# Performance work log

Measured on AMD Instinct MI355X. Metric: run time of the kernel, lower is better.

Reference implementation:

```python
import jax, jax.numpy as jnp
import numpy as np

N = 100000   # nodes
E = 3200000  # edges (avg degree 32)
WIDTH = 32
DEPTH = 4


def setup_inputs() -> dict:
    key = jax.random.key(0)
    ks = jax.random.split(key, 12)
    def lin(k, fan_in, fan_out):
        s = 1.0 / np.sqrt(fan_in)
        kw, kb = jax.random.split(k)
        W = jax.random.uniform(kw, (fan_in, fan_out), jnp.float32, -s, s)
        b = jax.random.uniform(kb, (fan_out,), jnp.float32, -s, s)
        return W, b
    x = jax.random.normal(ks[0], (N, 3), jnp.float32)
    edge_index = jax.random.randint(ks[1], (2, E), 0, N, jnp.int64)
    fc1_w, fc1_b = lin(ks[2], 3, WIDTH)
    w1, b1 = lin(ks[3], WIDTH, 2 * WIDTH)
    w2, b2 = lin(ks[4], 2 * WIDTH, 2 * WIDTH)
    w3, b3 = lin(ks[5], 2 * WIDTH, WIDTH)
    fc2_w, fc2_b = lin(ks[6], WIDTH, 1)
    return {"x": x, "edge_index": edge_index,
            "fc1_w": fc1_w, "fc1_b": fc1_b,
            "w1": w1, "b1": b1, "w2": w2, "b2": b2, "w3": w3, "b3": b3,
            "fc2_w": fc2_w, "fc2_b": fc2_b}


def reference(x, edge_index, fc1_w, fc1_b, w1, b1, w2, b2, w3, b3, fc2_w, fc2_b):
    # GCNConv semantics: add self-loops, symmetric degree normalization,
    # linear transform then normalized scatter-add aggregation.
    loops = jnp.arange(N, dtype=edge_index.dtype)
    src = jnp.concatenate([edge_index[0], loops])  # [E+N]
    dst = jnp.concatenate([edge_index[1], loops])  # [E+N]
    deg = jax.ops.segment_sum(jnp.ones_like(dst, dtype=x.dtype), dst, num_segments=N)
    dinv = jnp.where(deg > 0, jax.lax.rsqrt(deg), 0.0)
    norm = (dinv[src] * dinv[dst])[:, None]  # [E+N, 1]

    def gcn(h, W, b):
        m = (h @ W)[src] * norm                      # gather + scale
        return jax.ops.segment_sum(m, dst, num_segments=N) + b  # scatter-add

    h = x @ fc1_w + fc1_b
    for _ in range(DEPTH):
        h = jax.nn.relu(gcn(h, w1, b1))
        h = jax.nn.relu(gcn(h, w2, b2))
        h = jax.nn.relu(gcn(h, w3, b3))
    return h @ fc2_w + fc2_b
```

## Files before the change

kernel.cpp:

```cpp
#include <hip/hip_runtime.h>
#include <hip/hip_fp16.h>

constexpr int NN = 100000;
constexpr int EE = 3200000;
constexpr int BLOCK = 256;
constexpr int NBINS = 782;
constexpr int BINCAP = 5120;
constexpr int CHUNK = 4096;
constexpr int NCHB = (EE + CHUNK - 1) / CHUNK;
constexpr int NCLS = 512;

typedef _Float16 h2v __attribute__((ext_vector_type(2)));

__device__ __forceinline__ unsigned int pack2(float x, float y) {
  return __builtin_bit_cast(unsigned int, __floats2half2_rn(x, y));
}

__device__ __forceinline__ float dot2acc(float acc, unsigned int a, unsigned int b) {
#if __has_builtin(__builtin_amdgcn_fdot2)
  return __builtin_amdgcn_fdot2(__builtin_bit_cast(h2v, a),
                                __builtin_bit_cast(h2v, b), acc, false);
#else
  float2 fa = __half22float2(__builtin_bit_cast(__half2, a));
  float2 fb = __half22float2(__builtin_bit_cast(__half2, b));
  return fmaf(fa.x, fb.x, fmaf(fa.y, fb.y, acc));
#endif
}

__device__ __forceinline__ float addLo(float acc, unsigned int bits) {
#if __has_builtin(__builtin_amdgcn_fdot2)
  h2v h = __builtin_bit_cast(h2v, bits);
  const h2v eLo = {(_Float16)1.0f, (_Float16)0.0f};
  return __builtin_amdgcn_fdot2(h, eLo, acc, false);
#else
  __half2 hh = __builtin_bit_cast(__half2, bits);
  return acc + __half2float(hh.x);
#endif
}

__device__ __forceinline__ float addHi(float acc, unsigned int bits) {
#if __has_builtin(__builtin_amdgcn_fdot2)
  h2v h = __builtin_bit_cast(h2v, bits);
  const h2v eHi = {(_Float16)0.0f, (_Float16)1.0f};
  return __builtin_amdgcn_fdot2(h, eHi, acc, false);
#else
  __half2 hh = __builtin_bit_cast(__half2, bits);
  return acc + __half2float(hh.y);
#endif
}

__global__ __launch_bounds__(256) void k_binA(const int* __restrict__ src,
                                              const int* __restrict__ dst,
                                              int* __restrict__ cursor,
                                              unsigned int* __restrict__ binarr) {
  __shared__ int cnt[1024];
  __shared__ int off[1024];
  __shared__ int gbase[NBINS];
  __shared__ int ssc[256];
  __shared__ unsigned int stag[CHUNK];
  int tid = threadIdx.x;
  int base = blockIdx.x * CHUNK;
  for (int i = tid; i < 1024; i += 256) cnt[i] = 0;
  __syncthreads();
  for (int i = tid; i < CHUNK; i += 256) {
    int e = base + i;
    if (e < EE) atomicAdd(&cnt[dst[e] >> 7], 1);
  }
  __syncthreads();
  int t4 = tid * 4;
  int s0 = cnt[t4], s1 = cnt[t4 + 1], s2 = cnt[t4 + 2], s3 = cnt[t4 + 3];
  int tsum = s0 + s1 + s2 + s3;
  ssc[tid] = tsum;
  __syncthreads();
  for (int o = 1; o < 256; o <<= 1) {
    int x = (tid >= o) ? ssc[tid - o] : 0;
    __syncthreads();
    ssc[tid] += x;
    __syncthreads();
  }
  int ex = ssc[tid] - tsum;
  off[t4] = ex;
  off[t4 + 1] = ex + s0;
  off[t4 + 2] = ex + s0 + s1;
  off[t4 + 3] = ex + s0 + s1 + s2;
  __syncthreads();
  for (int b = tid; b < NBINS; b += 256) {
    int c = cnt[b];
    gbase[b] = c ? atomicAdd(&cursor[b], c) : 0;
    cnt[b] = off[b];
  }
  __syncthreads();
  for (int i = tid; i < CHUNK; i += 256) {
    int e = base + i;
    if (e < EE) {
      int d = dst[e];
      int b = d >> 7;
      int p = atomicAdd(&cnt[b], 1);
      stag[p] = ((unsigned int)src[e] << 7) | (unsigned int)(d & 127);
    }
  }
  __syncthreads();
  int total = (base + CHUNK <= EE) ? CHUNK : (EE - base);
  for (int i = tid; i < total; i += 256) {
    int lo = 0, hi = NBINS - 1;
    while (lo < hi) {
      int mid = (lo + hi + 1) >> 1;
      if (off[mid] <= i) lo = mid;
      else hi = mid - 1;
    }
    binarr[(size_t)lo * BINCAP + gbase[lo] + (i - off[lo])] = stag[i];
  }
}

__global__ __launch_bounds__(256) void k_degcnt(const unsigned int* __restrict__ binarr,
                                                const int* __restrict__ cursor,
                                                int* __restrict__ deg,
                                                int* __restrict__ bh) {
  __shared__ int cnt[128];
  __shared__ int lh[NCLS];
  int b = blockIdx.x, tid = threadIdx.x;
  if (tid < 128) cnt[tid] = 0;
  for (int i = tid; i < NCLS; i += 256) lh[i] = 0;
  __syncthreads();
  int n = cursor[b];
  const unsigned int* p = binarr + (size_t)b * BINCAP;
  for (int i = tid; i < n; i += 256) atomicAdd(&cnt[p[i] & 127], 1);
  __syncthreads();
  int node = b * 128 + tid;
  if (tid < 128 && node < NN) {
    int d = cnt[tid] < NCLS ? cnt[tid] : NCLS - 1;
    deg[node] = d;
    atomicAdd(&lh[d], 1);
  }
  __syncthreads();
  for (int i = tid; i < NCLS; i += 256) bh[(size_t)i * NBINS + b] = lh[i];
}

__global__ __launch_bounds__(256) void k_rowscan(int* __restrict__ bh,
                                                 int* __restrict__ tot) {
  int wid = (blockIdx.x * 256 + threadIdx.x) >> 6;
  int lane = threadIdx.x & 63;
  if (wid >= NCLS) return;
  int* row = bh + (size_t)wid * NBINS;
  int run = 0;
  for (int base = 0; base < NBINS; base += 64) {
    int i = base + lane;
    int v = (i < NBINS) ? row[i] : 0;
    int s = v;
#pragma unroll
    for (int o = 1; o < 64; o <<= 1) {
      int x = __shfl_up(s, o);
      if (lane >= o) s += x;
    }
    if (i < NBINS) row[i] = run + s - v;
    run += __shfl(s, 63);
  }
  if (lane == 0) tot[wid] = run;
}

__global__ __launch_bounds__(NCLS) void k_clsscan(const int* __restrict__ tot,
                                                  int* __restrict__ nodestart,
                                                  int* __restrict__ edgebase) {
  __shared__ int sn[NCLS], se[NCLS];
  int t = threadIdx.x;
  int v = tot[t];
  int e0 = v * t;
  sn[t] = v;
  se[t] = e0;
  __syncthreads();
  for (int o = 1; o < NCLS; o <<= 1) {
    int a = 0, b = 0;
    if (t >= o) { a = sn[t - o]; b = se[t - o]; }
    __syncthreads();
    if (t >= o) { sn[t] += a; se[t] += b; }
    __syncthreads();
  }
  nodestart[t] = sn[t] - v;
  edgebase[t] = se[t] - e0;
}

__global__ __launch_bounds__(256) void k_place2(const int* __restrict__ deg,
                                                const int* __restrict__ bh,
                                                const int* __restrict__ nodestart,
                                                const int* __restrict__ edgebase,
                                                int* __restrict__ perm,
                                                int* __restrict__ invp,
                                                int* __restrict__ rowptr2,
                                                float* __restrict__ dinv2) {
  __shared__ int lcur[NCLS];
  int tid = threadIdx.x, b = blockIdx.x;
  for (int i = tid; i < NCLS; i += 256)
    lcur[i] = nodestart[i] + bh[(size_t)i * NBINS + b];
  __syncthreads();
  int n = b * 128 + tid;
  if (tid >= 128 || n >= NN) return;
  int d = deg[n];
  int nid = atomicAdd(&lcur[d], 1);
  perm[nid] = n;
  invp[n] = nid;
  int idx = nid - nodestart[d];
  rowptr2[nid] = edgebase[d] + idx * d;
  dinv2[nid] = rsqrtf((float)(d + 1));
  if (n == 0) rowptr2[NN] = EE;
}

__global__ __launch_bounds__(256) void k_binB2(const unsigned int* __restrict__ binarr,
                                               const int* __restrict__ cursor,
                                               const int* __restrict__ invp,
                                               const int* __restrict__ rowptr2,
                                               int* __restrict__ col2) {
  __shared__ unsigned int stag[BINCAP];
  __shared__ unsigned int stag2[BINCAP];
  __shared__ int cnt[1024];
  __shared__ unsigned short off16[1024];
  __shared__ int nbase[128];
  __shared__ int ssc[256];
  int b = blockIdx.x, tid = threadIdx.x;
  int n = cursor[b];
  const unsigned int* p = binarr + (size_t)b * BINCAP;
  for (int i = tid; i < 1024; i += 256) cnt[i] = 0;
  int node = b * 128 + tid;
  if (tid < 128) nbase[tid] = (node < NN) ? rowptr2[invp[node]] : 0;
  __syncthreads();
  for (int i = tid; i < n; i += 256) {
    unsigned int e = p[i];
    unsigned int s = (unsigned int)invp[e >> 7];
    stag[i] = (s << 7) | (e & 127u);
    atomicAdd(&cnt[((e & 127u) << 3) | (s >> 14)], 1);
  }
  __syncthreads();
  int t4 = tid * 4;
  int s0 = cnt[t4], s1 = cnt[t4 + 1], s2 = cnt[t4 + 2], s3 = cnt[t4 + 3];
  int tsum = s0 + s1 + s2 + s3;
  ssc[tid] = tsum;
  __syncthreads();
  for (int o = 1; o < 256; o <<= 1) {
    int x = (tid >= o) ? ssc[tid - o] : 0;
    __syncthreads();
    ssc[tid] += x;
    __syncthreads();
  }
  int ex = ssc[tid] - tsum;
  off16[t4] = (unsigned short)ex;
  off16[t4 + 1] = (unsigned short)(ex + s0);
  off16[t4 + 2] = (unsigned short)(ex + s0 + s1);
  off16[t4 + 3] = (unsigned short)(ex + s0 + s1 + s2);
  cnt[t4] = ex;
  cnt[t4 + 1] = ex + s0;
  cnt[t4 + 2] = ex + s0 + s1;
  cnt[t4 + 3] = ex + s0 + s1 + s2;
  __syncthreads();
  for (int i = tid; i < n; i += 256) {
    unsigned int en = stag[i];
    int key = (int)(((en & 127u) << 3) | ((en >> 7) >> 14));
    int pos = atomicAdd(&cnt[key], 1);
    stag2[pos] = en;
  }
  __syncthreads();
  for (int i = tid; i < n; i += 256) {
    unsigned int en = stag2[i];
    int dl = (int)(en & 127u);
    col2[nbase[dl] + (i - (int)off16[dl << 3])] = (int)(en >> 7);
  }
}

__global__ __launch_bounds__(BLOCK) void k_fc1(const float* __restrict__ x,
                                               __half* __restrict__ t0,
                                               const float* __restrict__ W,
                                               const float* __restrict__ b,
                                               const float* __restrict__ dinv,
                                               const int* __restrict__ perm) {
  __shared__ float Ws[3 * 32];
  __shared__ float bs[32];
  int tid = threadIdx.x;
  if (tid < 96) Ws[tid] = W[tid];
  if (tid < 32) bs[tid] = b[tid];
  __syncthreads();
  int node = blockIdx.x * 8 + (tid >> 5);
  int f = tid & 31;
  if (node >= NN) return;
  int on = perm[node];
  float x0 = x[on * 3], x1 = x[on * 3 + 1], x2 = x[on * 3 + 2];
  float v = fmaf(x0, Ws[f], fmaf(x1, Ws[32 + f], fmaf(x2, Ws[64 + f], bs[f])));
  t0[node * 32 + f] = __float2half(v * dinv[node]);
}

__global__ __launch_bounds__(BLOCK) void k_A(const uint2* __restrict__ t0,
                                             __half2* __restrict__ t1,
                                             const int* __restrict__ rowptr,
                                             const int* __restrict__ col,
                                             const float* __restrict__ dinv,
                                             const float* __restrict__ W1,
                                             const float* __restrict__ b1) {
  __shared__ unsigned int W1p[16 * 64];
  __shared__ float b1s[64];
  __shared__ unsigned int Hs2[32 * 17];
  int tid = threadIdx.x;
  for (int i = tid; i < 16 * 64; i += BLOCK) {
    int k2 = i >> 6, j = i & 63;
    W1p[i] = pack2(W1[(2 * k2) * 64 + j], W1[(2 * k2 + 1) * 64 + j]);
  }
  if (tid < 64) b1s[tid] = b1[tid];
  __syncthreads();

  int tile = (int)gridDim.x - 1 - (int)blockIdx.x;
  {
    int c = tid & 7, slot = tid >> 3;
    int node = tile * 32 + slot;
    uint2 raw = t0[(size_t)node * 8 + c];
    float a0 = 0.f, a1 = 0.f, a2 = 0.f, a3 = 0.f;
    a0 = addLo(a0, raw.x); a1 = addHi(a1, raw.x);
    a2 = addLo(a2, raw.y); a3 = addHi(a3, raw.y);
    int beg = rowptr[node], end = rowptr[node + 1];
#pragma unroll 8
    for (int e = beg; e < end; ++e) {
      uint2 r = t0[(size_t)col[e] * 8 + c];
      a0 = addLo(a0, r.x); a1 = addHi(a1, r.x);
      a2 = addLo(a2, r.y); a3 = addHi(a3, r.y);
    }
    float dv = dinv[node];
    Hs2[slot * 17 + 2 * c] = pack2(a0 * dv, a1 * dv);
    Hs2[slot * 17 + 2 * c + 1] = pack2(a2 * dv, a3 * dv);
  }
  __syncthreads();
  {
    int n = tid >> 3, c8 = tid & 7;
    int node = tile * 32 + n;
    float a[8];
#pragma unroll
    for (int j = 0; j < 8; ++j) a[j] = b1s[c8 * 8 + j];
#pragma unroll
    for (int k2 = 0; k2 < 16; ++k2) {
      unsigned int h = Hs2[n * 17 + k2];
#pragma unroll
      for (int jj = 0; jj < 8; ++jj)
        a[jj] = dot2acc(a[jj], h, W1p[k2 * 64 + c8 * 8 + jj]);
    }
    float dv = dinv[node];
    __half2* o = t1 + (size_t)node * 32 + c8 * 4;
#pragma unroll
    for (int jj = 0; jj < 4; ++jj)
      o[jj] = __float22half2_rn(make_float2(fmaxf(a[2 * jj], 0.f) * dv,
                                            fmaxf(a[2 * jj + 1], 0.f) * dv));
  }
}

__global__ __launch_bounds__(BLOCK) void k_C(const uint2* __restrict__ t1,
                                             __half2* __restrict__ t3,
                                             const int* __restrict__ rowptr,
                                             const int* __restrict__ col,
                                             const float* __restrict__ dinv,
                                             const float* __restrict__ W2,
                                             const float* __restrict__ b2,
                                             const float* __restrict__ W3) {
  __shared__ unsigned int W2p[32 * 64];
  __shared__ unsigned int W3p[32 * 32];
  __shared__ float b2s[64];
  __shared__ unsigned int H2p[16 * 33];
  __shared__ unsigned int G1p[16 * 33];
  int tid = threadIdx.x;
  for (int i = tid; i < 32 * 64; i += BLOCK) {
    int k2 = i >> 6, j = i & 63;
    W2p[i] = pack2(W2[(2 * k2) * 64 + j], W2[(2 * k2 + 1) * 64 + j]);
  }
  for (int i = tid; i < 32 * 32; i += BLOCK) {
    int k2 = i >> 5, j = i & 31;
    W3p[i] = pack2(W3[(2 * k2) * 32 + j], W3[(2 * k2 + 1) * 32 + j]);
  }
  if (tid < 64) b2s[tid] = b2[tid];
  __syncthreads();

  int tile = (int)gridDim.x - 1 - (int)blockIdx.x;
  {
    int c = tid & 15, slot = tid >> 4;
    int node = tile * 16 + slot;
    uint2 raw = t1[(size_t)node * 16 + c];
    float a0 = 0.f, a1 = 0.f, a2 = 0.f, a3 = 0.f;
    a0 = addLo(a0, raw.x); a1 = addHi(a1, raw.x);
    a2 = addLo(a2, raw.y); a3 = addHi(a3, raw.y);
    int beg = rowptr[node], end = rowptr[node + 1];
#pragma unroll 8
    for (int e = beg; e < end; ++e) {
      uint2 r = t1[(size_t)col[e] * 16 + c];
      a0 = addLo(a0, r.x); a1 = addHi(a1, r.x);
      a2 = addLo(a2, r.y); a3 = addHi(a3, r.y);
    }
    float dv = dinv[node];
    H2p[slot * 33 + 2 * c] = pack2(a0 * dv, a1 * dv);
    H2p[slot * 33 + 2 * c + 1] = pack2(a2 * dv, a3 * dv);
  }
  __syncthreads();
  {
    int n = tid >> 4, q = tid & 15;
    float a[4];
#pragma unroll
    for (int j = 0; j < 4; ++j) a[j] = b2s[q * 4 + j];
#pragma unroll
    for (int k2 = 0; k2 < 32; ++k2) {
      unsigned int h = H2p[n * 33 + k2];
#pragma unroll
      for (int jj = 0; jj < 4; ++jj)
        a[jj] = dot2acc(a[jj], h, W2p[k2 * 64 + q * 4 + jj]);
    }
    G1p[n * 33 + q * 2] = pack2(fmaxf(a[0], 0.f), fmaxf(a[1], 0.f));
    G1p[n * 33 + q * 2 + 1] = pack2(fmaxf(a[2], 0.f), fmaxf(a[3], 0.f));
  }
  __syncthreads();
  {
    int n = tid >> 4, c16 = tid & 15;
    int node = tile * 16 + n;
    float a0 = 0.f, a1 = 0.f;
#pragma unroll
    for (int k2 = 0; k2 < 32; ++k2) {
      unsigned int g = G1p[n * 33 + k2];
      a0 = dot2acc(a0, g, W3p[k2 * 32 + 2 * c16]);
      a1 = dot2acc(a1, g, W3p[k2 * 32 + 2 * c16 + 1]);
    }
    float dv = dinv[node];
    t3[(size_t)node * 16 + c16] = __float22half2_rn(make_float2(a0 * dv, a1 * dv));
  }
}

template <bool FINAL>
__global__ __launch_bounds__(BLOCK) void k_D(const uint2* __restrict__ t3,
                                             uint2* __restrict__ t0n,
                                             float* __restrict__ out,
                                             const int* __restrict__ rowptr,
                                             const int* __restrict__ col,
                                             const float* __restrict__ dinv,
                                             const float* __restrict__ b3,
                                             const float* __restrict__ fc2w,
                                             const float* __restrict__ fc2b,
                                             const int* __restrict__ perm) {
  int tid = threadIdx.x;
  int c = tid & 7, slot = tid >> 3;
  int tile = (int)gridDim.x - 1 - (int)blockIdx.x;
  int node = tile * 32 + slot;
  uint2 raw = t3[(size_t)node * 8 + c];
  float a0 = 0.f, a1 = 0.f, a2 = 0.f, a3 = 0.f;
  a0 = addLo(a0, raw.x); a1 = addHi(a1, raw.x);
  a2 = addLo(a2, raw.y); a3 = addHi(a3, raw.y);
  int beg = rowptr[node], end = rowptr[node + 1];
#pragma unroll 8
  for (int e = beg; e < end; ++e) {
    uint2 r = t3[(size_t)col[e] * 8 + c];
    a0 = addLo(a0, r.x); a1 = addHi(a1, r.x);
    a2 = addLo(a2, r.y); a3 = addHi(a3, r.y);
  }
  float dv = dinv[node];
  float h0 = fmaxf(fmaf(a0, dv, b3[4 * c]), 0.f);
  float h1 = fmaxf(fmaf(a1, dv, b3[4 * c + 1]), 0.f);
  float h2 = fmaxf(fmaf(a2, dv, b3[4 * c + 2]), 0.f);
  float h3 = fmaxf(fmaf(a3, dv, b3[4 * c + 3]), 0.f);
  if (!FINAL) {
    uint2 w;
    w.x = pack2(h0 * dv, h1 * dv);
    w.y = pack2(h2 * dv, h3 * dv);
    t0n[(size_t)node * 8 + c] = w;
  } else {
    float part = fmaf(h0, fc2w[4 * c],
                 fmaf(h1, fc2w[4 * c + 1],
                 fmaf(h2, fc2w[4 * c + 2], h3 * fc2w[4 * c + 3])));
#pragma unroll
    for (int off = 4; off > 0; off >>= 1) part += __shfl_down(part, off, 8);
    if (c == 0) out[perm[node]] = part + fc2b[0];
  }
}

extern "C" void kernel_launch(void* const* d_in, const int* in_sizes, int n_in,
                              void* d_out, int out_size, void* d_ws, size_t ws_size,
                              hipStream_t stream) {
  const float* x = (const float*)d_in[0];
  const int* ei = (const int*)d_in[1];
  const int* esrc = ei;
  const int* edst = ei + EE;
  const float* fc1_w = (const float*)d_in[2];
  const float* fc1_b = (const float*)d_in[3];
  const float* w1 = (const float*)d_in[4];
  const float* b1 = (const float*)d_in[5];
  const float* w2 = (const float*)d_in[6];
  const float* b2 = (const float*)d_in[7];
  const float* w3 = (const float*)d_in[8];
  const float* b3 = (const float*)d_in[9];
  const float* fc2_w = (const float*)d_in[10];
  const float* fc2_b = (const float*)d_in[11];

  char* p = (char*)d_ws;
  auto carve = [&](size_t bytes) {
    void* r = (void*)p;
    p += (bytes + 255) & ~(size_t)255;
    return r;
  };
  int* cursor = (int*)carve(NBINS * sizeof(int));
  int* nodestart = (int*)carve(NCLS * sizeof(int));
  int* edgebase = (int*)carve(NCLS * sizeof(int));
  int* tot = (int*)carve(NCLS * sizeof(int));
  int* deg = (int*)carve(NN * sizeof(int));
  int* bh = (int*)carve((size_t)NCLS * NBINS * sizeof(int));
  unsigned int* binarr = (unsigned int*)carve((size_t)NBINS * BINCAP * 4);
  int* rowptr2 = (int*)carve((NN + 1) * sizeof(int));
  int* col2 = (int*)carve(EE * sizeof(int));
  int* perm = (int*)carve(NN * sizeof(int));
  int* invp = (int*)carve(NN * sizeof(int));
  float* dinv2 = (float*)carve(NN * sizeof(float));
  __half* t32a = (__half*)carve((size_t)NN * 32 * sizeof(__half));
  __half* t64 = (__half*)carve((size_t)NN * 64 * sizeof(__half));
  __half* t32b = (__half*)carve((size_t)NN * 32 * sizeof(__half));

  hipMemsetAsync(cursor, 0, NBINS * sizeof(int), stream);

  k_binA<<<NCHB, 256, 0, stream>>>(esrc, edst, cursor, binarr);
  k_degcnt<<<NBINS, 256, 0, stream>>>(binarr, cursor, deg, bh);
  k_rowscan<<<(NCLS * 64 + 255) / 256, 256, 0, stream>>>(bh, tot);
  k_clsscan<<<1, NCLS, 0, stream>>>(tot, nodestart, edgebase);
  k_place2<<<NBINS, 256, 0, stream>>>(deg, bh, nodestart, edgebase, perm, invp,
                                      rowptr2, dinv2);
  k_binB2<<<NBINS, 256, 0, stream>>>(binarr, cursor, invp, rowptr2, col2);

  k_fc1<<<NN / 8, BLOCK, 0, stream>>>(x, t32a, fc1_w, fc1_b, dinv2, perm);

  for (int it = 0; it < 4; ++it) {
    k_A<<<NN / 32, BLOCK, 0, stream>>>((const uint2*)t32a, (__half2*)t64,
                                       rowptr2, col2, dinv2, w1, b1);
    k_C<<<NN / 16, BLOCK, 0, stream>>>((const uint2*)t64, (__half2*)t32b,
                                       rowptr2, col2, dinv2, w2, b2, w3);
    if (it < 3) {
      k_D<false><<<NN / 32, BLOCK, 0, stream>>>(
          (const uint2*)t32b, (uint2*)t32a, nullptr, rowptr2, col2, dinv2, b3,
          nullptr, nullptr, nullptr);
    } else {
      k_D<true><<<NN / 32, BLOCK, 0, stream>>>(
          (const uint2*)t32b, nullptr, (float*)d_out, rowptr2, col2, dinv2, b3,
          fc2_w, fc2_b, perm);
    }
  }
}
```

Before: 638.5 us.

## Use 16-byte gathers with split-edge halves in aggregation kernels and simplify binning

The three aggregation kernels now gather each neighbour row with uint4 (16-byte) loads instead of uint2. Each node's edge list is split across two thread groups that take alternating edges, and their partial sums are combined with a cross-lane shuffle. This is meant to cut the number of load instructions per edge and raise memory-level parallelism in the gather-bound loops. Separately, k_binA moves to 512 threads, records each staged edge's bin id in shared memory so the binary search can go away, and merges the cursor atomics into the scan step. The cost is more accumulator registers, extra shuffles, and possible imbalance between the two halves on odd-degree nodes.

```diff
diff --git a/kernel.cpp b/kernel.cpp
--- a/kernel.cpp
+++ b/kernel.cpp
@@ -49,66 +49,65 @@
 #endif
 }
 
-__global__ __launch_bounds__(256) void k_binA(const int* __restrict__ src,
+#define ACC8(r)                                                     \
+  a0 = addLo(a0, (r).x); a1 = addHi(a1, (r).x);                     \
+  a2 = addLo(a2, (r).y); a3 = addHi(a3, (r).y);                     \
+  a4 = addLo(a4, (r).z); a5 = addHi(a5, (r).z);                     \
+  a6 = addLo(a6, (r).w); a7 = addHi(a7, (r).w)
+
+__global__ __launch_bounds__(512) void k_binA(const int* __restrict__ src,
                                               const int* __restrict__ dst,
                                               int* __restrict__ cursor,
                                               unsigned int* __restrict__ binarr) {
   __shared__ int cnt[1024];
   __shared__ int off[1024];
   __shared__ int gbase[NBINS];
-  __shared__ int ssc[256];
+  __shared__ int ssc[512];
   __shared__ unsigned int stag[CHUNK];
+  __shared__ unsigned short binid[CHUNK];
   int tid = threadIdx.x;
   int base = blockIdx.x * CHUNK;
-  for (int i = tid; i < 1024; i += 256) cnt[i] = 0;
-  __syncthreads();
-  for (int i = tid; i < CHUNK; i += 256) {
+  for (int i = tid; i < 1024; i += 512) cnt[i] = 0;
+  __syncthreads();
+  for (int i = tid; i < CHUNK; i += 512) {
     int e = base + i;
     if (e < EE) atomicAdd(&cnt[dst[e] >> 7], 1);
   }
   __syncthreads();
-  int t4 = tid * 4;
-  int s0 = cnt[t4], s1 = cnt[t4 + 1], s2 = cnt[t4 + 2], s3 = cnt[t4 + 3];
-  int tsum = s0 + s1 + s2 + s3;
+  int t2 = tid * 2;
+  int s0 = cnt[t2], s1 = cnt[t2 + 1];
+  int tsum = s0 + s1;
   ssc[tid] = tsum;
   __syncthreads();
-  for (int o = 1; o < 256; o <<= 1) {
+  for (int o = 1; o < 512; o <<= 1) {
     int x = (tid >= o) ? ssc[tid - o] : 0;
     __syncthreads();
     ssc[tid] += x;
     __syncthreads();
   }
   int ex = ssc[tid] - tsum;
-  off[t4] = ex;
-  off[t4 + 1] = ex + s0;
-  off[t4 + 2] = ex + s0 + s1;
-  off[t4 + 3] = ex + s0 + s1 + s2;
-  __syncthreads();
-  for (int b = tid; b < NBINS; b += 256) {
-    int c = cnt[b];
-    gbase[b] = c ? atomicAdd(&cursor[b], c) : 0;
-    cnt[b] = off[b];
-  }
-  __syncthreads();
-  for (int i = tid; i < CHUNK; i += 256) {
+  off[t2] = ex;
+  off[t2 + 1] = ex + s0;
+  cnt[t2] = ex;
+  cnt[t2 + 1] = ex + s0;
+  if (t2 < NBINS) gbase[t2] = s0 ? atomicAdd(&cursor[t2], s0) : 0;
+  if (t2 + 1 < NBINS) gbase[t2 + 1] = s1 ? atomicAdd(&cursor[t2 + 1], s1) : 0;
+  __syncthreads();
+  for (int i = tid; i < CHUNK; i += 512) {
     int e = base + i;
     if (e < EE) {
       int d = dst[e];
       int b = d >> 7;
       int p = atomicAdd(&cnt[b], 1);
       stag[p] = ((unsigned int)src[e] << 7) | (unsigned int)(d & 127);
+      binid[p] = (unsigned short)b;
     }
   }
   __syncthreads();
   int total = (base + CHUNK <= EE) ? CHUNK : (EE - base);
-  for (int i = tid; i < total; i += 256) {
-    int lo = 0, hi = NBINS - 1;
-    while (lo < hi) {
-      int mid = (lo + hi + 1) >> 1;
-      if (off[mid] <= i) lo = mid;
-      else hi = mid - 1;
-    }
-    binarr[(size_t)lo * BINCAP + gbase[lo] + (i - off[lo])] = stag[i];
+  for (int i = tid; i < total; i += 512) {
+    int b = binid[i];
+    binarr[(size_t)b * BINCAP + gbase[b] + (i - off[b])] = stag[i];
   }
 }
 
@@ -285,7 +284,7 @@
   t0[node * 32 + f] = __float2half(v * dinv[node]);
 }
 
-__global__ __launch_bounds__(BLOCK) void k_A(const uint2* __restrict__ t0,
+__global__ __launch_bounds__(BLOCK) void k_A(const uint4* __restrict__ t0,
                                              __half2* __restrict__ t1,
                                              const int* __restrict__ rowptr,
                                              const int* __restrict__ col,
@@ -305,22 +304,33 @@
 
   int tile = (int)gridDim.x - 1 - (int)blockIdx.x;
   {
-    int c = tid & 7, slot = tid >> 3;
+    int c = tid & 3;
+    int half = (tid >> 2) & 1;
+    int slot = tid >> 3;
     int node = tile * 32 + slot;
-    uint2 raw = t0[(size_t)node * 8 + c];
     float a0 = 0.f, a1 = 0.f, a2 = 0.f, a3 = 0.f;
-    a0 = addLo(a0, raw.x); a1 = addHi(a1, raw.x);
-    a2 = addLo(a2, raw.y); a3 = addHi(a3, raw.y);
+    float a4 = 0.f, a5 = 0.f, a6 = 0.f, a7 = 0.f;
+    if (half == 0) {
+      uint4 raw = t0[(size_t)node * 4 + c];
+      ACC8(raw);
+    }
     int beg = rowptr[node], end = rowptr[node + 1];
-#pragma unroll 8
-    for (int e = beg; e < end; ++e) {
-      uint2 r = t0[(size_t)col[e] * 8 + c];
-      a0 = addLo(a0, r.x); a1 = addHi(a1, r.x);
-      a2 = addLo(a2, r.y); a3 = addHi(a3, r.y);
-    }
-    float dv = dinv[node];
-    Hs2[slot * 17 + 2 * c] = pack2(a0 * dv, a1 * dv);
-    Hs2[slot * 17 + 2 * c + 1] = pack2(a2 * dv, a3 * dv);
+#pragma unroll 4
+    for (int e = beg + half; e < end; e += 2) {
+      uint4 r = t0[(size_t)col[e] * 4 + c];
+      ACC8(r);
+    }
+    a0 += __shfl_xor(a0, 4); a1 += __shfl_xor(a1, 4);
+    a2 += __shfl_xor(a2, 4); a3 += __shfl_xor(a3, 4);
+    a4 += __shfl_xor(a4, 4); a5 += __shfl_xor(a5, 4);
+    a6 += __shfl_xor(a6, 4); a7 += __shfl_xor(a7, 4);
+    if (half == 0) {
+      float dv = dinv[node];
+      Hs2[slot * 17 + 4 * c] = pack2(a0 * dv, a1 * dv);
+      Hs2[slot * 17 + 4 * c + 1] = pack2(a2 * dv, a3 * dv);
+      Hs2[slot * 17 + 4 * c + 2] = pack2(a4 * dv, a5 * dv);
+      Hs2[slot * 17 + 4 * c + 3] = pack2(a6 * dv, a7 * dv);
+    }
   }
   __syncthreads();
   {
@@ -345,7 +355,7 @@
   }
 }
 
-__global__ __launch_bounds__(BLOCK) void k_C(const uint2* __restrict__ t1,
+__global__ __launch_bounds__(BLOCK) void k_C(const uint4* __restrict__ t1,
                                              __half2* __restrict__ t3,
                                              const int* __restrict__ rowptr,
                                              const int* __restrict__ col,
@@ -372,22 +382,33 @@
 
   int tile = (int)gridDim.x - 1 - (int)blockIdx.x;
   {
-    int c = tid & 15, slot = tid >> 4;
+    int c = tid & 7;
+    int half = (tid >> 3) & 1;
+    int slot = tid >> 4;
     int node = tile * 16 + slot;
-    uint2 raw = t1[(size_t)node * 16 + c];
     float a0 = 0.f, a1 = 0.f, a2 = 0.f, a3 = 0.f;
-    a0 = addLo(a0, raw.x); a1 = addHi(a1, raw.x);
-    a2 = addLo(a2, raw.y); a3 = addHi(a3, raw.y);
+    float a4 = 0.f, a5 = 0.f, a6 = 0.f, a7 = 0.f;
+    if (half == 0) {
+      uint4 raw = t1[(size_t)node * 8 + c];
+      ACC8(raw);
+    }
     int beg = rowptr[node], end = rowptr[node + 1];
-#pragma unroll 8
-    for (int e = beg; e < end; ++e) {
-      uint2 r = t1[(size_t)col[e] * 16 + c];
-      a0 = addLo(a0, r.x); a1 = addHi(a1, r.x);
-      a2 = addLo(a2, r.y); a3 = addHi(a3, r.y);
-    }
-    float dv = dinv[node];
-    H2p[slot * 33 + 2 * c] = pack2(a0 * dv, a1 * dv);
-    H2p[slot * 33 + 2 * c + 1] = pack2(a2 * dv, a3 * dv);
+#pragma unroll 4
+    for (int e = beg + half; e < end; e += 2) {
+      uint4 r = t1[(size_t)col[e] * 8 + c];
+      ACC8(r);
+    }
+    a0 += __shfl_xor(a0, 8); a1 += __shfl_xor(a1, 8);
+    a2 += __shfl_xor(a2, 8); a3 += __shfl_xor(a3, 8);
+    a4 += __shfl_xor(a4, 8); a5 += __shfl_xor(a5, 8);
+    a6 += __shfl_xor(a6, 8); a7 += __shfl_xor(a7, 8);
+    if (half == 0) {
+      float dv = dinv[node];
+      H2p[slot * 33 + 4 * c] = pack2(a0 * dv, a1 * dv);
+      H2p[slot * 33 + 4 * c + 1] = pack2(a2 * dv, a3 * dv);
+      H2p[slot * 33 + 4 * c + 2] = pack2(a4 * dv, a5 * dv);
+      H2p[slot * 33 + 4 * c + 3] = pack2(a6 * dv, a7 * dv);
+    }
   }
   __syncthreads();
   {
@@ -422,8 +443,8 @@
 }
 
 template <bool FINAL>
-__global__ __launch_bounds__(BLOCK) void k_D(const uint2* __restrict__ t3,
-                                             uint2* __restrict__ t0n,
+__global__ __launch_bounds__(BLOCK) void k_D(const uint4* __restrict__ t3,
+                                             uint4* __restrict__ t0n,
                                              float* __restrict__ out,
                                              const int* __restrict__ rowptr,
                                              const int* __restrict__ col,
@@ -433,37 +454,56 @@
                                              const float* __restrict__ fc2b,
                                              const int* __restrict__ perm) {
   int tid = threadIdx.x;
-  int c = tid & 7, slot = tid >> 3;
+  int c = tid & 3;
+  int half = (tid >> 2) & 1;
+  int slot = tid >> 3;
   int tile = (int)gridDim.x - 1 - (int)blockIdx.x;
   int node = tile * 32 + slot;
-  uint2 raw = t3[(size_t)node * 8 + c];
   float a0 = 0.f, a1 = 0.f, a2 = 0.f, a3 = 0.f;
-  a0 = addLo(a0, raw.x); a1 = addHi(a1, raw.x);
-  a2 = addLo(a2, raw.y); a3 = addHi(a3, raw.y);
+  float a4 = 0.f, a5 = 0.f, a6 = 0.f, a7 = 0.f;
+  if (half == 0) {
+    uint4 raw = t3[(size_t)node * 4 + c];
+    ACC8(raw);
+  }
   int beg = rowptr[node], end = rowptr[node + 1];
-#pragma unroll 8
-  for (int e = beg; e < end; ++e) {
-    uint2 r = t3[(size_t)col[e] * 8 + c];
-    a0 = addLo(a0, r.x); a1 = addHi(a1, r.x);
-    a2 = addLo(a2, r.y); a3 = addHi(a3, r.y);
-  }
+#pragma unroll 4
+  for (int e = beg + half; e < end; e += 2) {
+    uint4 r = t3[(size_t)col[e] * 4 + c];
+    ACC8(r);
+  }
+  a0 += __shfl_xor(a0, 4); a1 += __shfl_xor(a1, 4);
+  a2 += __shfl_xor(a2, 4); a3 += __shfl_xor(a3, 4);
+  a4 += __shfl_xor(a4, 4); a5 += __shfl_xor(a5, 4);
+  a6 += __shfl_xor(a6, 4); a7 += __shfl_xor(a7, 4);
   float dv = dinv[node];
-  float h0 = fmaxf(fmaf(a0, dv, b3[4 * c]), 0.f);
-  float h1 = fmaxf(fmaf(a1, dv, b3[4 * c + 1]), 0.f);
-  float h2 = fmaxf(fmaf(a2, dv, b3[4 * c + 2]), 0.f);
-  float h3 = fmaxf(fmaf(a3, dv, b3[4 * c + 3]), 0.f);
+  float h0 = fmaxf(fmaf(a0, dv, b3[8 * c]), 0.f);
+  float h1 = fmaxf(fmaf(a1, dv, b3[8 * c + 1]), 0.f);
+  float h2 = fmaxf(fmaf(a2, dv, b3[8 * c + 2]), 0.f);
+  float h3 = fmaxf(fmaf(a3, dv, b3[8 * c + 3]), 0.f);
+  float h4 = fmaxf(fmaf(a4, dv, b3[8 * c + 4]), 0.f);
+  float h5 = fmaxf(fmaf(a5, dv, b3[8 * c + 5]), 0.f);
+  float h6 = fmaxf(fmaf(a6, dv, b3[8 * c + 6]), 0.f);
+  float h7 = fmaxf(fmaf(a7, dv, b3[8 * c + 7]), 0.f);
   if (!FINAL) {
-    uint2 w;
-    w.x = pack2(h0 * dv, h1 * dv);
-    w.y = pack2(h2 * dv, h3 * dv);
-    t0n[(size_t)node * 8 + c] = w;
+    if (half == 0) {
+      uint4 w;
+      w.x = pack2(h0 * dv, h1 * dv);
+      w.y = pack2(h2 * dv, h3 * dv);
+      w.z = pack2(h4 * dv, h5 * dv);
+      w.w = pack2(h6 * dv, h7 * dv);
+      t0n[(size_t)node * 4 + c] = w;
+    }
   } else {
-    float part = fmaf(h0, fc2w[4 * c],
-                 fmaf(h1, fc2w[4 * c + 1],
-                 fmaf(h2, fc2w[4 * c + 2], h3 * fc2w[4 * c + 3])));
-#pragma unroll
-    for (int off = 4; off > 0; off >>= 1) part += __shfl_down(part, off, 8);
-    if (c == 0) out[perm[node]] = part + fc2b[0];
+    float part = fmaf(h0, fc2w[8 * c],
+                 fmaf(h1, fc2w[8 * c + 1],
+                 fmaf(h2, fc2w[8 * c + 2],
+                 fmaf(h3, fc2w[8 * c + 3],
+                 fmaf(h4, fc2w[8 * c + 4],
+                 fmaf(h5, fc2w[8 * c + 5],
+                 fmaf(h6, fc2w[8 * c + 6], h7 * fc2w[8 * c + 7])))))));
+    part += __shfl_xor(part, 1);
+    part += __shfl_xor(part, 2);
+    if ((tid & 7) == 0) out[perm[node]] = part + fc2b[0];
   }
 }
 
@@ -509,7 +549,7 @@
 
   hipMemsetAsync(cursor, 0, NBINS * sizeof(int), stream);
 
-  k_binA<<<NCHB, 256, 0, stream>>>(esrc, edst, cursor, binarr);
+  k_binA<<<NCHB, 512, 0, stream>>>(esrc, edst, cursor, binarr);
   k_degcnt<<<NBINS, 256, 0, stream>>>(binarr, cursor, deg, bh);
   k_rowscan<<<(NCLS * 64 + 255) / 256, 256, 0, stream>>>(bh, tot);
   k_clsscan<<<1, NCLS, 0, stream>>>(tot, nodestart, edgebase);
@@ -520,17 +560,17 @@
   k_fc1<<<NN / 8, BLOCK, 0, stream>>>(x, t32a, fc1_w, fc1_b, dinv2, perm);
 
   for (int it = 0; it < 4; ++it) {
-    k_A<<<NN / 32, BLOCK, 0, stream>>>((const uint2*)t32a, (__half2*)t64,
+    k_A<<<NN / 32, BLOCK, 0, stream>>>((const uint4*)t32a, (__half2*)t64,
                                        rowptr2, col2, dinv2, w1, b1);
-    k_C<<<NN / 16, BLOCK, 0, stream>>>((const uint2*)t64, (__half2*)t32b,
+    k_C<<<NN / 16, BLOCK, 0, stream>>>((const uint4*)t64, (__half2*)t32b,
                                        rowptr2, col2, dinv2, w2, b2, w3);
     if (it < 3) {
       k_D<false><<<NN / 32, BLOCK, 0, stream>>>(
-          (const uint2*)t32b, (uint2*)t32a, nullptr, rowptr2, col2, dinv2, b3,
+          (const uint4*)t32b, (uint4*)t32a, nullptr, rowptr2, col2, dinv2, b3,
           nullptr, nullptr, nullptr);
     } else {
       k_D<true><<<NN / 32, BLOCK, 0, stream>>>(
-          (const uint2*)t32b, nullptr, (float*)d_out, rowptr2, col2, dinv2, b3,
+          (const uint4*)t32b, nullptr, (float*)d_out, rowptr2, col2, dinv2, b3,
           fc2_w, fc2_b, perm);
     }
   }
```

Result: faster. 599.0 us, median of 2 (-6.2%).
